# Kernel tuning notes

Measured on AMD Instinct MI355X. Metric: run time of the kernel, lower is better.

Reference implementation:

```python
import jax, jax.numpy as jnp
import numpy as np

B, S, H = 2, 2048, 1024
N, DK = 16, 64          # heads, key/value dim (N*DK == H)
DF = 4096               # FFN hidden
SCALE = 1.0 / float(DK) ** 0.5
EPS = 1e-5


def _layer_norm(x, g, b):
    mu = jnp.mean(x, axis=-1, keepdims=True)
    var = jnp.var(x, axis=-1, keepdims=True)
    return (x - mu) * jax.lax.rsqrt(var + EPS) * g + b


def setup_inputs() -> dict:
    key = jax.random.key(0)
    ks = jax.random.split(key, 12)
    s = 0.02
    return {
        "x": jax.random.normal(ks[0], (B, S, H), dtype=jnp.float32),
        "Wq": jax.random.normal(ks[1], (N * DK, H), dtype=jnp.float32) * s,
        "bq": jnp.zeros((N * DK,), jnp.float32),
        "Wk": jax.random.normal(ks[2], (N * DK, H), dtype=jnp.float32) * s,
        "bk": jnp.zeros((N * DK,), jnp.float32),
        "Wv": jax.random.normal(ks[3], (N * DK, H), dtype=jnp.float32) * s,
        "bv": jnp.zeros((N * DK,), jnp.float32),
        "Wo": jax.random.normal(ks[4], (H, N * DK), dtype=jnp.float32) * s,
        "bo": jnp.zeros((H,), jnp.float32),
        "W1": jax.random.normal(ks[5], (DF, H), dtype=jnp.float32) * s,
        "b1": jnp.zeros((DF,), jnp.float32),
        "W2": jax.random.normal(ks[6], (H, DF), dtype=jnp.float32) * s,
        "b2": jnp.zeros((H,), jnp.float32),
        "ln1_g": jnp.ones((H,), jnp.float32),
        "ln1_b": jnp.zeros((H,), jnp.float32),
        "ln2_g": jnp.ones((H,), jnp.float32),
        "ln2_b": jnp.zeros((H,), jnp.float32),
    }


def _mha(x, Wq, bq, Wk, bk, Wv, bv, Wo, bo):
    b = x.shape[0]
    q = (x @ Wq.T + bq).reshape(b, -1, N, DK)  # [B,T,N,DK]
    k = (x @ Wk.T + bk).reshape(b, -1, N, DK)
    v = (x @ Wv.T + bv).reshape(b, -1, N, DK)
    # naive full-score attention, faithful to torch einsum layout
    scores = jnp.einsum('btnd,bsnd->tsbn', q, k) * SCALE  # [T,S,B,N]
    p = jax.nn.softmax(scores, axis=1)                    # softmax over S (dim=1)
    attn = jnp.einsum('tsbn,bsnd->btnd', p, v)            # [B,T,N,DK]
    attn = attn.reshape(b, attn.shape[1], -1)             # [B,T,N*DK]
    return attn @ Wo.T + bo


def reference(x, Wq, bq, Wk, bk, Wv, bv, Wo, bo, W1, b1, W2, b2,
              ln1_g, ln1_b, ln2_g, ln2_b):
    # post-LN encoder layer: x = LN(x + MHA(x)); x = LN(x + FFN(x))
    h = _layer_norm(x + _mha(x, Wq, bq, Wk, bk, Wv, bv, Wo, bo), ln1_g, ln1_b)
    ff = jax.nn.relu(h @ W1.T + b1) @ W2.T + b2
    return _layer_norm(h + ff, ln2_g, ln2_b)
```

## Files before the change

### kernel.cpp

```cpp
#include <hip/hip_runtime.h>
#include <stdint.h>


typedef unsigned short u16;
typedef __bf16 bf16x8 __attribute__((ext_vector_type(8)));
typedef float  f32x4  __attribute__((ext_vector_type(4)));

__device__ __forceinline__ u16 f2bf(float f) {
    unsigned int u = __float_as_uint(f);
    u += 0x7FFFu + ((u >> 16) & 1u);
    return (u16)(u >> 16);
}

__device__ __forceinline__ float bf2f(u16 v) {
    return __uint_as_float((unsigned)v << 16);
}

__device__ __forceinline__ unsigned pack_bf16_hi(float lo, float hi) {
#if __has_builtin(__builtin_amdgcn_perm)
    return __builtin_amdgcn_perm(__float_as_uint(hi), __float_as_uint(lo), 0x07060302u);
#else
    return (__float_as_uint(lo) >> 16) | (__float_as_uint(hi) & 0xFFFF0000u);
#endif
}

__device__ __forceinline__ void async_load16(const u16* g, u16* l) {
    __builtin_amdgcn_global_load_lds(
        (__attribute__((address_space(1))) void*)g,
        (__attribute__((address_space(3))) void*)l, 16, 0, 0);
}

struct CvtArgs {
    const float* src[7];
    u16*         dst[7];
    int          n[7];
};

__global__ __launch_bounds__(256) void k_cvt_all(CvtArgs a) {
    const int seg = blockIdx.y;
    const int i = (blockIdx.x * 256 + threadIdx.x) * 8;
    if (i >= a.n[seg]) return;
    const float* in = a.src[seg];
    u16* out = a.dst[seg];
    float4 x = *(const float4*)(in + i);
    float4 y = *(const float4*)(in + i + 4);
    uint4 o;
    o.x = (unsigned)f2bf(x.x) | ((unsigned)f2bf(x.y) << 16);
    o.y = (unsigned)f2bf(x.z) | ((unsigned)f2bf(x.w) << 16);
    o.z = (unsigned)f2bf(y.x) | ((unsigned)f2bf(y.y) << 16);
    o.w = (unsigned)f2bf(y.z) | ((unsigned)f2bf(y.w) << 16);
    *(uint4*)(out + i) = o;
}

__global__ __launch_bounds__(256) void k_concat3(const float* __restrict__ a,
                                                 const float* __restrict__ b,
                                                 const float* __restrict__ c,
                                                 float* __restrict__ out) {
    int i = blockIdx.x * 256 + threadIdx.x;
    if (i >= 3072) return;
    out[i] = (i < 1024) ? a[i] : (i < 2048 ? b[i - 1024] : c[i - 2048]);
}

template<int OUT_BF16, int RELU>
__global__ __launch_bounds__(256, 4) void k_gemm_bt(
    const u16* __restrict__ A, const u16* __restrict__ Bw,
    const float* __restrict__ bias, void* __restrict__ Y,
    int M, int N, int K)
{
    __shared__ u16 As[128 * 64];
    __shared__ u16 Bs[128 * 64];
    const int tid  = threadIdx.x;
    const int wave = tid >> 6, lane = tid & 63;
    const int lm = lane & 15, lq = lane >> 4;
    const int m0 = blockIdx.x * 128, n0 = blockIdx.y * 128;
    const int wr = (wave >> 1) * 64, wc = (wave & 1) * 64;

    const int ksz = K / gridDim.z;
    const int ks  = blockIdx.z * ksz, ke = ks + ksz;

    const int sr8 = wave * 8 + (lane >> 3);
    const int scx = ((lane & 7) * 8) ^ (((sr8 >> 2) & 3) << 4);
    const size_t arow = (size_t)(m0 + sr8) * K + scx;
    const size_t brow = (size_t)(n0 + sr8) * K + scx;
    const int sw = ((lm >> 2) & 3) << 4;

    f32x4 acc[4][4];
#pragma unroll
    for (int i = 0; i < 4; i++)
#pragma unroll
        for (int j = 0; j < 4; j++) acc[i][j] = (f32x4){0.f, 0.f, 0.f, 0.f};

    for (int k0 = ks; k0 < ke; k0 += 64) {
        __syncthreads();
#pragma unroll
        for (int j = 0; j < 4; j++) {
            async_load16(A  + arow + (size_t)(j * 32) * K + k0, As + j * 2048 + wave * 512);
            async_load16(Bw + brow + (size_t)(j * 32) * K + k0, Bs + j * 2048 + wave * 512);
        }
        __syncthreads();

#pragma unroll
        for (int h = 0; h < 2; h++) {
            const int cofs = (h * 32 + lq * 8) ^ sw;
            bf16x8 af[4], bf[4];
#pragma unroll
            for (int i = 0; i < 4; i++)
                af[i] = *(const bf16x8*)(As + (wr + i * 16 + lm) * 64 + cofs);
#pragma unroll
            for (int j = 0; j < 4; j++)
                bf[j] = *(const bf16x8*)(Bs + (wc + j * 16 + lm) * 64 + cofs);
#pragma unroll
            for (int i = 0; i < 4; i++)
#pragma unroll
                for (int j = 0; j < 4; j++)
                    acc[i][j] = __builtin_amdgcn_mfma_f32_16x16x32_bf16(af[i], bf[j], acc[i][j], 0, 0, 0);
        }
    }

    const float bsc = (blockIdx.z == 0) ? 1.f : 0.f;
    const size_t zoff = (size_t)blockIdx.z * M * N;
#pragma unroll
    for (int i = 0; i < 4; i++) {
        const int mg = m0 + wr + i * 16 + lq * 4;
#pragma unroll
        for (int j = 0; j < 4; j++) {
            const int ng = n0 + wc + j * 16 + lm;
            const float bv = bias[ng] * bsc;
#pragma unroll
            for (int r = 0; r < 4; r++) {
                float v = acc[i][j][r] + bv;
                if (RELU) v = fmaxf(v, 0.f);
                if (OUT_BF16) ((u16*)Y)[zoff + (size_t)(mg + r) * N + ng] = f2bf(v);
                else          ((float*)Y)[zoff + (size_t)(mg + r) * N + ng] = v;
            }
        }
    }
}

__global__ __launch_bounds__(256) void k_transpose_v(const u16* __restrict__ qkv,
                                                     u16* __restrict__ vt) {
    __shared__ u16 T[64 * 72];
    const int tid = threadIdx.x;
    const int t0 = blockIdx.x * 64;
    const int bn = blockIdx.y;
    const int b = bn >> 4, n = bn & 15;
    {
        const int r = tid >> 2, c = (tid & 3) * 16;
        const u16* src = qkv + (size_t)(b * 2048 + t0 + r) * 3072 + 2048 + n * 64 + c;
        *(uint4*)&T[r * 72 + c]     = *(const uint4*)(src);
        *(uint4*)&T[r * 72 + c + 8] = *(const uint4*)(src + 8);
    }
    __syncthreads();
    {
        const int d = tid >> 2, c = (tid & 3) * 16;
        union { u16 h[16]; uint4 v[2]; } tmp;
#pragma unroll
        for (int j = 0; j < 16; j++) {
            const int w = c + j;
            const int k = ((w & 3) << 4) + (w >> 2);
            tmp.h[j] = T[k * 72 + d];
        }
        u16* dst = vt + (size_t)(bn * 64 + d) * 2048 + t0 + c;
        *(uint4*)(dst)     = tmp.v[0];
        *(uint4*)(dst + 8) = tmp.v[1];
    }
}

__global__ __launch_bounds__(256, 2) void k_flash(const u16* __restrict__ qkv,
                                                  const u16* __restrict__ vt,
                                                  u16* __restrict__ attn) {
    __shared__ u16 Ks[64 * 72];
    __shared__ u16 Vs[64 * 72];
    __shared__ u16 Ps[4 * 32 * 72];
    const int tid = threadIdx.x, wave = tid >> 6, lane = tid & 63;
    const int lm = lane & 15, lq = lane >> 4;
    const int b = blockIdx.z, n = blockIdx.y, qt0 = blockIdx.x * 128;

    bf16x8 qf[2][2];
#pragma unroll
    for (int mh = 0; mh < 2; mh++) {
        const u16* qp = qkv + (size_t)(b * 2048 + qt0 + wave * 32 + mh * 16 + lm) * 3072
                        + n * 64 + lq * 8;
        const bf16x8 q0r = *(const bf16x8*)(qp);
        const bf16x8 q1r = *(const bf16x8*)(qp + 32);
#pragma unroll
        for (int j = 0; j < 8; j++) {
            qf[mh][0][j] = (__bf16)((float)q0r[j] * 0.18033688f);
            qf[mh][1][j] = (__bf16)((float)q1r[j] * 0.18033688f);
        }
    }

    float lsum[2][4];
    f32x4 oacc[2][4];
#pragma unroll
    for (int mh = 0; mh < 2; mh++)
#pragma unroll
        for (int r = 0; r < 4; r++) { lsum[mh][r] = 0.f; }
#pragma unroll
    for (int mh = 0; mh < 2; mh++)
#pragma unroll
        for (int dt = 0; dt < 4; dt++) oacc[mh][dt] = (f32x4){0.f, 0.f, 0.f, 0.f};

    const int sr = tid >> 2, sc = (tid & 3) * 16;
    const u16* kg = qkv + (size_t)(b * 2048 + sr) * 3072 + 1024 + n * 64 + sc;
    const u16* vg = vt + (size_t)((b * 16 + n) * 64 + sr) * 2048 + sc;
    u16* PsW = Ps + wave * 32 * 72;

    uint4 kr0 = *(const uint4*)(kg);
    uint4 kr1 = *(const uint4*)(kg + 8);
    uint4 vr0 = *(const uint4*)(vg);
    uint4 vr1 = *(const uint4*)(vg + 8);

    for (int kt = 0; kt < 2048; kt += 64) {
        __syncthreads();
        *(uint4*)&Ks[sr * 72 + sc]     = kr0;
        *(uint4*)&Ks[sr * 72 + sc + 8] = kr1;
        *(uint4*)&Vs[sr * 72 + sc]     = vr0;
        *(uint4*)&Vs[sr * 72 + sc + 8] = vr1;
        __syncthreads();

        if (kt + 64 < 2048) {
            kr0 = *(const uint4*)(kg + (size_t)(kt + 64) * 3072);
            kr1 = *(const uint4*)(kg + (size_t)(kt + 64) * 3072 + 8);
            vr0 = *(const uint4*)(vg + kt + 64);
            vr1 = *(const uint4*)(vg + kt + 64 + 8);
        }

        f32x4 sf[2][4];
#pragma unroll
        for (int nt = 0; nt < 4; nt++) {
            const bf16x8 kf0 = *(const bf16x8*)(Ks + (nt * 16 + lm) * 72 + lq * 8);
            const bf16x8 kf1 = *(const bf16x8*)(Ks + (nt * 16 + lm) * 72 + lq * 8 + 32);
#pragma unroll
            for (int mh = 0; mh < 2; mh++) {
                f32x4 z = (f32x4){0.f, 0.f, 0.f, 0.f};
                z = __builtin_amdgcn_mfma_f32_16x16x32_bf16(qf[mh][0], kf0, z, 0, 0, 0);
                z = __builtin_amdgcn_mfma_f32_16x16x32_bf16(qf[mh][1], kf1, z, 0, 0, 0);
                sf[mh][nt] = z;
            }
        }

#pragma unroll
        for (int mh = 0; mh < 2; mh++)
#pragma unroll
            for (int r = 0; r < 4; r++) {
                const float p0 = __builtin_amdgcn_exp2f(sf[mh][0][r]);
                const float p1 = __builtin_amdgcn_exp2f(sf[mh][1][r]);
                const float p2 = __builtin_amdgcn_exp2f(sf[mh][2][r]);
                const float p3 = __builtin_amdgcn_exp2f(sf[mh][3][r]);
                lsum[mh][r] += (p0 + p1) + (p2 + p3);
                uint2 w;
                w.x = pack_bf16_hi(p0, p1);
                w.y = pack_bf16_hi(p2, p3);
                *(uint2*)&PsW[(mh * 16 + lq * 4 + r) * 72 + lm * 4] = w;
            }

#pragma unroll
        for (int s2 = 0; s2 < 2; s2++) {
            bf16x8 pf[2];
#pragma unroll
            for (int mh = 0; mh < 2; mh++)
                pf[mh] = *(const bf16x8*)(PsW + (mh * 16 + lm) * 72 + s2 * 32 + lq * 8);
#pragma unroll
            for (int dt = 0; dt < 4; dt++) {
                const bf16x8 vf = *(const bf16x8*)(Vs + (dt * 16 + lm) * 72 + s2 * 32 + lq * 8);
#pragma unroll
                for (int mh = 0; mh < 2; mh++)
                    oacc[mh][dt] = __builtin_amdgcn_mfma_f32_16x16x32_bf16(pf[mh], vf, oacc[mh][dt], 0, 0, 0);
            }
        }
    }

#pragma unroll
    for (int mh = 0; mh < 2; mh++)
#pragma unroll
        for (int r = 0; r < 4; r++) {
#pragma unroll
            for (int off = 8; off >= 1; off >>= 1)
                lsum[mh][r] += __shfl_xor(lsum[mh][r], off, 16);
            lsum[mh][r] = 1.f / lsum[mh][r];
        }
#pragma unroll
    for (int mh = 0; mh < 2; mh++)
#pragma unroll
        for (int dt = 0; dt < 4; dt++)
#pragma unroll
            for (int r = 0; r < 4; r++) {
                const float o = oacc[mh][dt][r] * lsum[mh][r];
                attn[(size_t)(b * 2048 + qt0 + wave * 32 + mh * 16 + lq * 4 + r) * 1024
                     + n * 64 + dt * 16 + lm] = f2bf(o);
            }
}

template<int WRITE_BF16>
__global__ __launch_bounds__(256) void k_ln_p4(const float* __restrict__ a,
                                               const u16* __restrict__ pb,
                                               const float* __restrict__ g,
                                               const float* __restrict__ be,
                                               float* __restrict__ outf,
                                               u16* __restrict__ outb) {
    const int row = blockIdx.x, tid = threadIdx.x;
    const size_t base = (size_t)row * 1024 + tid * 4;
    const float4 av = *(const float4*)(a + base);
    float x0 = av.x, x1 = av.y, x2 = av.z, x3 = av.w;
#pragma unroll
    for (int z = 0; z < 4; z++) {
        const uint2 w = *(const uint2*)(pb + (size_t)z * 4096 * 1024 + base);
        x0 += __uint_as_float(w.x << 16);
        x1 += __uint_as_float(w.x & 0xFFFF0000u);
        x2 += __uint_as_float(w.y << 16);
        x3 += __uint_as_float(w.y & 0xFFFF0000u);
    }
    float s1 = x0 + x1 + x2 + x3;
    float s2 = x0 * x0 + x1 * x1 + x2 * x2 + x3 * x3;
#pragma unroll
    for (int off = 32; off >= 1; off >>= 1) {
        s1 += __shfl_down(s1, off);
        s2 += __shfl_down(s2, off);
    }
    __shared__ float red[8];
    __shared__ float stats[2];
    const int wave = tid >> 6, lane = tid & 63;
    if (lane == 0) { red[wave] = s1; red[4 + wave] = s2; }
    __syncthreads();
    if (tid == 0) {
        const float t1 = red[0] + red[1] + red[2] + red[3];
        const float t2 = red[4] + red[5] + red[6] + red[7];
        const float mean = t1 * (1.f / 1024.f);
        const float var = t2 * (1.f / 1024.f) - mean * mean;
        stats[0] = mean;
        stats[1] = rsqrtf(var + 1e-5f);
    }
    __syncthreads();
    const float mean = stats[0], rstd = stats[1];
    const int c = tid * 4;
    const float4 gv = *(const float4*)(g + c);
    const float4 bev = *(const float4*)(be + c);
    float4 y;
    y.x = (x0 - mean) * rstd * gv.x + bev.x;
    y.y = (x1 - mean) * rstd * gv.y + bev.y;
    y.z = (x2 - mean) * rstd * gv.z + bev.z;
    y.w = (x3 - mean) * rstd * gv.w + bev.w;
    *(float4*)(outf + base) = y;
    if (WRITE_BF16) {
        uint2 o;
        o.x = (unsigned)f2bf(y.x) | ((unsigned)f2bf(y.y) << 16);
        o.y = (unsigned)f2bf(y.z) | ((unsigned)f2bf(y.w) << 16);
        *(uint2*)(outb + base) = o;
    }
}

extern "C" void kernel_launch(void* const* d_in, const int* in_sizes, int n_in,
                              void* d_out, int out_size, void* d_ws, size_t ws_size,
                              hipStream_t stream) {
    const float* x   = (const float*)d_in[0];
    const float* Wq  = (const float*)d_in[1];
    const float* bq  = (const float*)d_in[2];
    const float* Wk  = (const float*)d_in[3];
    const float* bk  = (const float*)d_in[4];
    const float* Wv  = (const float*)d_in[5];
    const float* bv  = (const float*)d_in[6];
    const float* Wo  = (const float*)d_in[7];
    const float* bo  = (const float*)d_in[8];
    const float* W1  = (const float*)d_in[9];
    const float* b1  = (const float*)d_in[10];
    const float* W2  = (const float*)d_in[11];
    const float* b2  = (const float*)d_in[12];
    const float* g1  = (const float*)d_in[13];
    const float* be1 = (const float*)d_in[14];
    const float* g2  = (const float*)d_in[15];
    const float* be2 = (const float*)d_in[16];

    char* ws = (char*)d_ws;
    const size_t MB = 1024 * 1024;
    u16*   wqkv = (u16*)(ws + 0);
    u16*   wo_b = (u16*)(ws + 6 * MB);
    u16*   w1_b = (u16*)(ws + 8 * MB);
    u16*   w2_b = (u16*)(ws + 16 * MB);
    float* bqkv = (float*)(ws + 24 * MB);
    u16*   xb   = (u16*)(ws + 25 * MB);
    u16*   qkv  = (u16*)(ws + 33 * MB);
    u16*   vt   = (u16*)(ws + 57 * MB);
    u16*   attn = (u16*)(ws + 65 * MB);
    u16*   op4  = (u16*)(ws + 33 * MB);
    float* h    = (float*)(ws + 65 * MB);
    u16*   hb   = (u16*)(ws + 81 * MB);
    u16*   ff1  = (u16*)(ws + 33 * MB);
    u16*   fp4  = (u16*)(ws + 81 * MB);

    CvtArgs ca;
    ca.src[0] = x;  ca.dst[0] = xb;                  ca.n[0] = 4096 * 1024;
    ca.src[1] = Wq; ca.dst[1] = wqkv;                ca.n[1] = 1024 * 1024;
    ca.src[2] = Wk; ca.dst[2] = wqkv + 1024 * 1024;  ca.n[2] = 1024 * 1024;
    ca.src[3] = Wv; ca.dst[3] = wqkv + 2 * 1024 * 1024; ca.n[3] = 1024 * 1024;
    ca.src[4] = Wo; ca.dst[4] = wo_b;                ca.n[4] = 1024 * 1024;
    ca.src[5] = W1; ca.dst[5] = w1_b;                ca.n[5] = 4096 * 1024;
    ca.src[6] = W2; ca.dst[6] = w2_b;                ca.n[6] = 4096 * 1024;
    k_cvt_all<<<dim3(2048, 7), 256, 0, stream>>>(ca);
    k_concat3<<<12, 256, 0, stream>>>(bq, bk, bv, bqkv);

    k_gemm_bt<1, 0><<<dim3(32, 24), 256, 0, stream>>>(
        xb, wqkv, bqkv, qkv, 4096, 3072, 1024);

    k_transpose_v<<<dim3(32, 32), 256, 0, stream>>>(qkv, vt);

    k_flash<<<dim3(16, 16, 2), 256, 0, stream>>>(qkv, vt, attn);

    k_gemm_bt<1, 0><<<dim3(32, 8, 4), 256, 0, stream>>>(
        attn, wo_b, bo, op4, 4096, 1024, 1024);

    k_ln_p4<1><<<4096, 256, 0, stream>>>(x, op4, g1, be1, h, hb);

    k_gemm_bt<1, 1><<<dim3(32, 32), 256, 0, stream>>>(
        hb, w1_b, b1, ff1, 4096, 4096, 1024);

    k_gemm_bt<1, 0><<<dim3(32, 8, 4), 256, 0, stream>>>(
        ff1, w2_b, b2, fp4, 4096, 1024, 4096);

    k_ln_p4<0><<<4096, 256, 0, stream>>>(h, fp4, g2, be2, (float*)d_out, nullptr);
}
```

Baseline: 326.2 us.

## Double-buffer K/V tiles in flash kernel and raise MFMA wave priority

Splits the shared K and V tiles into two buffers, so the next tile is written into the idle buffer while the current one is consumed. This cuts the loop from two barriers per iteration to one and prefetches global data two tiles ahead. It also wraps the MFMA sections in s_setprio to favour matrix-issue waves. In exchange it doubles K/V LDS usage, which could affect occupancy, and holds more prefetch registers live.

```diff
diff --git a/kernel.cpp b/kernel.cpp
--- a/kernel.cpp
+++ b/kernel.cpp
@@ -169,8 +169,8 @@
 __global__ __launch_bounds__(256, 2) void k_flash(const u16* __restrict__ qkv,
                                                   const u16* __restrict__ vt,
                                                   u16* __restrict__ attn) {
-    __shared__ u16 Ks[64 * 72];
-    __shared__ u16 Vs[64 * 72];
+    __shared__ u16 Ks[2][64 * 72];
+    __shared__ u16 Vs[2][64 * 72];
     __shared__ u16 Ps[4 * 32 * 72];
     const int tid = threadIdx.x, wave = tid >> 6, lane = tid & 63;
     const int lm = lane & 15, lq = lane >> 4;
@@ -206,31 +206,48 @@
     const u16* vg = vt + (size_t)((b * 16 + n) * 64 + sr) * 2048 + sc;
     u16* PsW = Ps + wave * 32 * 72;
 
-    uint4 kr0 = *(const uint4*)(kg);
-    uint4 kr1 = *(const uint4*)(kg + 8);
-    uint4 vr0 = *(const uint4*)(vg);
-    uint4 vr1 = *(const uint4*)(vg + 8);
-
+    {
+        uint4 a0 = *(const uint4*)(kg);
+        uint4 a1 = *(const uint4*)(kg + 8);
+        uint4 b0 = *(const uint4*)(vg);
+        uint4 b1 = *(const uint4*)(vg + 8);
+        *(uint4*)&Ks[0][sr * 72 + sc]     = a0;
+        *(uint4*)&Ks[0][sr * 72 + sc + 8] = a1;
+        *(uint4*)&Vs[0][sr * 72 + sc]     = b0;
+        *(uint4*)&Vs[0][sr * 72 + sc + 8] = b1;
+    }
+    uint4 kr0 = *(const uint4*)(kg + 3072);
+    uint4 kr1 = *(const uint4*)(kg + 3072 + 8);
+    uint4 vr0 = *(const uint4*)(vg + 64);
+    uint4 vr1 = *(const uint4*)(vg + 64 + 8);
+    __syncthreads();
+
+    int c = 0;
     for (int kt = 0; kt < 2048; kt += 64) {
-        __syncthreads();
-        *(uint4*)&Ks[sr * 72 + sc]     = kr0;
-        *(uint4*)&Ks[sr * 72 + sc + 8] = kr1;
-        *(uint4*)&Vs[sr * 72 + sc]     = vr0;
-        *(uint4*)&Vs[sr * 72 + sc + 8] = vr1;
-        __syncthreads();
-
         if (kt + 64 < 2048) {
-            kr0 = *(const uint4*)(kg + (size_t)(kt + 64) * 3072);
-            kr1 = *(const uint4*)(kg + (size_t)(kt + 64) * 3072 + 8);
-            vr0 = *(const uint4*)(vg + kt + 64);
-            vr1 = *(const uint4*)(vg + kt + 64 + 8);
-        }
+            u16* Kd = Ks[c ^ 1];
+            u16* Vd = Vs[c ^ 1];
+            *(uint4*)&Kd[sr * 72 + sc]     = kr0;
+            *(uint4*)&Kd[sr * 72 + sc + 8] = kr1;
+            *(uint4*)&Vd[sr * 72 + sc]     = vr0;
+            *(uint4*)&Vd[sr * 72 + sc + 8] = vr1;
+            if (kt + 128 < 2048) {
+                kr0 = *(const uint4*)(kg + (size_t)(kt + 128) * 3072);
+                kr1 = *(const uint4*)(kg + (size_t)(kt + 128) * 3072 + 8);
+                vr0 = *(const uint4*)(vg + kt + 128);
+                vr1 = *(const uint4*)(vg + kt + 128 + 8);
+            }
+        }
+
+        const u16* Kc = Ks[c];
+        const u16* Vc = Vs[c];
 
         f32x4 sf[2][4];
+        __builtin_amdgcn_s_setprio(1);
 #pragma unroll
         for (int nt = 0; nt < 4; nt++) {
-            const bf16x8 kf0 = *(const bf16x8*)(Ks + (nt * 16 + lm) * 72 + lq * 8);
-            const bf16x8 kf1 = *(const bf16x8*)(Ks + (nt * 16 + lm) * 72 + lq * 8 + 32);
+            const bf16x8 kf0 = *(const bf16x8*)(Kc + (nt * 16 + lm) * 72 + lq * 8);
+            const bf16x8 kf1 = *(const bf16x8*)(Kc + (nt * 16 + lm) * 72 + lq * 8 + 32);
 #pragma unroll
             for (int mh = 0; mh < 2; mh++) {
                 f32x4 z = (f32x4){0.f, 0.f, 0.f, 0.f};
@@ -239,6 +256,7 @@
                 sf[mh][nt] = z;
             }
         }
+        __builtin_amdgcn_s_setprio(0);
 
 #pragma unroll
         for (int mh = 0; mh < 2; mh++)
@@ -255,6 +273,7 @@
                 *(uint2*)&PsW[(mh * 16 + lq * 4 + r) * 72 + lm * 4] = w;
             }
 
+        __builtin_amdgcn_s_setprio(1);
 #pragma unroll
         for (int s2 = 0; s2 < 2; s2++) {
             bf16x8 pf[2];
@@ -263,12 +282,16 @@
                 pf[mh] = *(const bf16x8*)(PsW + (mh * 16 + lm) * 72 + s2 * 32 + lq * 8);
 #pragma unroll
             for (int dt = 0; dt < 4; dt++) {
-                const bf16x8 vf = *(const bf16x8*)(Vs + (dt * 16 + lm) * 72 + s2 * 32 + lq * 8);
+                const bf16x8 vf = *(const bf16x8*)(Vc + (dt * 16 + lm) * 72 + s2 * 32 + lq * 8);
 #pragma unroll
                 for (int mh = 0; mh < 2; mh++)
                     oacc[mh][dt] = __builtin_amdgcn_mfma_f32_16x16x32_bf16(pf[mh], vf, oacc[mh][dt], 0, 0, 0);
             }
         }
+        __builtin_amdgcn_s_setprio(0);
+
+        __syncthreads();
+        c ^= 1;
     }
 
 #pragma unroll
```

Result: slower. 339.0 us, median of 2 (+3.9%).
